# Kernel optimization log

Measured on AMD Instinct MI355X. Metric: run time of the kernel, lower is better.

## Reference

```python
import jax, jax.numpy as jnp
import numpy as np

M, D, I, E, TOPK = 2048, 1024, 2048, 8, 2

def setup_inputs() -> dict:
    key = jax.random.key(0)
    k1, k2, k3, k4 = jax.random.split(key, 4)
    x = jax.random.normal(k1, (M, D), dtype=jnp.float32)
    w13 = jax.random.normal(k2, (E, 2 * I, D), dtype=jnp.float32) * 0.02
    w2 = jax.random.normal(k3, (E, D, I), dtype=jnp.float32) * 0.02
    expert_indices = jax.random.randint(k4, (M, TOPK), 0, E, dtype=jnp.int64)
    return {"x": x, "w13": w13, "w2": w2, "expert_indices": expert_indices}

def reference(x, w13, w2, expert_indices):
    # Faithful to the 'gpt-fast' math: per (token, slot) SiLU-gated expert FFN.
    # Instead of gathering per-token weight copies (huge), compute each expert's
    # FFN densely over all tokens, then gather the selected expert output.
    inter = w2.shape[2]

    def per_expert(w13_e, w2_e):
        h = jnp.einsum('md,nd->mn', x, w13_e)          # [M, 2I]
        x1, x3 = h[:, :inter], h[:, inter:]
        return jnp.einsum('mi,di->md', jax.nn.silu(x1) * x3, w2_e)  # [M, D]

    outs = jax.vmap(per_expert)(w13, w2)               # [E, M, D]
    outs = jnp.transpose(outs, (1, 0, 2))              # [M, E, D]
    # out[t, a] = outs[t, expert_indices[t, a]]
    idx = expert_indices[..., None]                    # [M, TOPK, 1]
    return jnp.take_along_axis(outs, idx, axis=1)      # [M, TOPK, D]
```

## Files before the change

kernel.cpp:

```cpp
#include <hip/hip_runtime.h>
#include <hip/hip_bf16.h>
#include <cstdint>
#include <cstddef>

#define DDIM  1024
#define IDIM  2048
#define NEXP  8
#define NPAIR 4096
#define KSPLIT 4
#define MAXTILE 40

typedef __attribute__((ext_vector_type(8))) short short8;
typedef __attribute__((ext_vector_type(4))) float floatx4;
typedef __attribute__((ext_vector_type(4))) float fvec4;

__device__ inline short8 pack8(float4 a, float4 b) {
    union { short8 s8; __hip_bfloat162 h[4]; } u;
    u.h[0] = __float22bfloat162_rn(float2{a.x, a.y});
    u.h[1] = __float22bfloat162_rn(float2{a.z, a.w});
    u.h[2] = __float22bfloat162_rn(float2{b.x, b.y});
    u.h[3] = __float22bfloat162_rn(float2{b.z, b.w});
    return u.s8;
}

__device__ inline short8 pack8v(fvec4 a, fvec4 b) {
    union { short8 s8; __hip_bfloat162 h[4]; } u;
    u.h[0] = __float22bfloat162_rn(float2{a.x, a.y});
    u.h[1] = __float22bfloat162_rn(float2{a.z, a.w});
    u.h[2] = __float22bfloat162_rn(float2{b.x, b.y});
    u.h[3] = __float22bfloat162_rn(float2{b.z, b.w});
    return u.s8;
}

__device__ inline void gload_lds16(const unsigned short* g, unsigned short* l) {
    __builtin_amdgcn_global_load_lds((const __attribute__((address_space(1))) void*)g,
                                     (__attribute__((address_space(3))) void*)l, 16, 0, 0);
}

__launch_bounds__(256)
__global__ void cvt_all(const fvec4* __restrict__ x, const fvec4* __restrict__ w13,
                        const fvec4* __restrict__ w2,
                        uint4* __restrict__ xb, uint4* __restrict__ w13b,
                        uint4* __restrict__ w2b) {
    const int t = threadIdx.x;
    for (int job = blockIdx.x; job < 6400; job += gridDim.x) {
        const fvec4* src; uint4* dst; int cbase;
        if (job < 4096)      { src = w13; dst = w13b; cbase = job << 10; }
        else if (job < 6144) { src = w2;  dst = w2b;  cbase = (job - 4096) << 10; }
        else                 { src = x;   dst = xb;   cbase = (job - 6144) << 10; }
        const int c0 = cbase + t;
        fvec4 a0 = __builtin_nontemporal_load(src + 2 * (c0 + 0));
        fvec4 b0 = __builtin_nontemporal_load(src + 2 * (c0 + 0) + 1);
        fvec4 a1 = __builtin_nontemporal_load(src + 2 * (c0 + 256));
        fvec4 b1 = __builtin_nontemporal_load(src + 2 * (c0 + 256) + 1);
        fvec4 a2 = __builtin_nontemporal_load(src + 2 * (c0 + 512));
        fvec4 b2 = __builtin_nontemporal_load(src + 2 * (c0 + 512) + 1);
        fvec4 a3 = __builtin_nontemporal_load(src + 2 * (c0 + 768));
        fvec4 b3 = __builtin_nontemporal_load(src + 2 * (c0 + 768) + 1);
        __builtin_amdgcn_sched_barrier(0);
        short8 p0 = pack8v(a0, b0);
        short8 p1 = pack8v(a1, b1);
        short8 p2 = pack8v(a2, b2);
        short8 p3 = pack8v(a3, b3);
        dst[c0 + 0]   = *(uint4*)&p0;
        dst[c0 + 256] = *(uint4*)&p1;
        dst[c0 + 512] = *(uint4*)&p2;
        dst[c0 + 768] = *(uint4*)&p3;
    }
}

__global__ void route_kernel(const int* __restrict__ eidx,
                             int4* __restrict__ tbl,
                             int* __restrict__ slot_q) {
    __shared__ int cnt[NEXP];
    __shared__ int cur[NEXP];
    const int t = threadIdx.x;
    if (t < NEXP) cnt[t] = 0;
    __syncthreads();
    for (int q = t; q < NPAIR; q += 1024) atomicAdd(&cnt[eidx[q]], 1);
    __syncthreads();
    if (t == 0) {
        int s = 0, nt = 0;
        for (int e = 0; e < NEXP; e++) {
            cur[e] = s;
            for (int mb = 0; mb < cnt[e]; mb += 128)
                tbl[nt++] = int4{e, mb, s, cnt[e]};
            s += cnt[e];
        }
        for (; nt < MAXTILE; nt++) tbl[nt] = int4{0, 0, 0, 0};
    }
    __syncthreads();
    for (int q = t; q < NPAIR; q += 1024) {
        int e = eidx[q];
        int pos = atomicAdd(&cur[e], 1);
        slot_q[pos] = q;
    }
}

__launch_bounds__(256)
__global__ void gemm1_swiglu(const unsigned short* __restrict__ xb,
                             const unsigned short* __restrict__ w13b,
                             const int4* __restrict__ tbl,
                             const int* __restrict__ slot_q,
                             unsigned short* __restrict__ pbuf) {
    const int4 tt = tbl[blockIdx.y];
    const int e = tt.x, mbase = tt.y, off0 = tt.z, ne = tt.w;
    if (mbase >= ne) return;
    const int n0 = blockIdx.x * 64;

    __shared__ __align__(16) unsigned short As[128 * 64];
    __shared__ __align__(16) unsigned short Bs[128 * 64];

    const int t    = threadIdx.x;
    const int lane = t & 63;
    const int wid  = t >> 6;

    const int rr = t >> 3;
    const int g  = (t & 7) ^ (rr & 7);
    const unsigned short* pA[4];
    const unsigned short* pB[4];
    const unsigned short* wb1 = w13b + (size_t)e * (2 * IDIM) * DDIM;
    #pragma unroll
    for (int c = 0; c < 4; c++) {
        int row = c * 32 + rr;
        int sl = mbase + row; if (sl > ne - 1) sl = ne - 1;
        pA[c] = xb + (size_t)(slot_q[off0 + sl] >> 1) * DDIM + g * 8;
        int wrow = (row < 64) ? (n0 + row) : (IDIM + n0 + (row - 64));
        pB[c] = wb1 + (size_t)wrow * DDIM + g * 8;
    }
    unsigned short* lA = As + wid * 512;
    unsigned short* lB = Bs + wid * 512;

    const int wm = wid >> 1, wn = wid & 1;
    const int quad = lane >> 4, l16 = lane & 15;
    const int rsw = l16 & 7;
    const int co0 = (quad ^ rsw) * 8;
    const int co1 = ((quad + 4) ^ rsw) * 8;

    floatx4 acc1[4][2], acc3[4][2];
    #pragma unroll
    for (int i = 0; i < 4; i++)
        #pragma unroll
        for (int j = 0; j < 2; j++) {
            acc1[i][j] = floatx4{0.f, 0.f, 0.f, 0.f};
            acc3[i][j] = floatx4{0.f, 0.f, 0.f, 0.f};
        }

    for (int it = 0; it < DDIM / 64; ++it) {
        const int ko = it * 64;
        __syncthreads();
        #pragma unroll
        for (int c = 0; c < 4; c++) {
            gload_lds16(pA[c] + ko, lA + c * 2048);
            gload_lds16(pB[c] + ko, lB + c * 2048);
        }
        __syncthreads();

        #pragma unroll
        for (int h = 0; h < 2; ++h) {
            const int co = h ? co1 : co0;
            short8 af[4], b1f[2], b3f[2];
            #pragma unroll
            for (int mi = 0; mi < 4; mi++)
                af[mi] = *(short8*)&As[(wm * 64 + mi * 16 + l16) * 64 + co];
            #pragma unroll
            for (int ni = 0; ni < 2; ni++) {
                b1f[ni] = *(short8*)&Bs[(wn * 32 + ni * 16 + l16) * 64 + co];
                b3f[ni] = *(short8*)&Bs[(64 + wn * 32 + ni * 16 + l16) * 64 + co];
            }
            #pragma unroll
            for (int mi = 0; mi < 4; mi++)
                #pragma unroll
                for (int ni = 0; ni < 2; ni++) {
                    acc1[mi][ni] = __builtin_amdgcn_mfma_f32_16x16x32_bf16(af[mi], b1f[ni], acc1[mi][ni], 0, 0, 0);
                    acc3[mi][ni] = __builtin_amdgcn_mfma_f32_16x16x32_bf16(af[mi], b3f[ni], acc3[mi][ni], 0, 0, 0);
                }
        }
    }

    #pragma unroll
    for (int mi = 0; mi < 4; mi++) {
        #pragma unroll
        for (int ni = 0; ni < 2; ni++) {
            const int col = n0 + wn * 32 + ni * 16 + l16;
            #pragma unroll
            for (int rw = 0; rw < 4; rw++) {
                const int s2 = mbase + wm * 64 + mi * 16 + quad * 4 + rw;
                if (s2 < ne) {
                    float v1 = acc1[mi][ni][rw];
                    float v3 = acc3[mi][ni][rw];
                    float pv = v1 / (1.f + __expf(-v1)) * v3;
                    __hip_bfloat16 pb = __float2bfloat16(pv);
                    pbuf[(size_t)(off0 + s2) * IDIM + col] = *(unsigned short*)&pb;
                }
            }
        }
    }
}

__launch_bounds__(256)
__global__ void gemm2_scatter(const unsigned short* __restrict__ pbuf,
                              const unsigned short* __restrict__ w2b,
                              const int4* __restrict__ tbl,
                              const int* __restrict__ slot_q,
                              float* __restrict__ parts) {
    const int4 tt = tbl[blockIdx.y];
    const int e = tt.x, mbase = tt.y, off0 = tt.z, ne = tt.w;
    if (mbase >= ne) return;
    const int n0 = blockIdx.x * 128;
    const int kbase = blockIdx.z * (IDIM / KSPLIT);
    float* dstbase = parts + (size_t)blockIdx.z * NPAIR * DDIM;

    __shared__ __align__(16) unsigned short As[128 * 64];
    __shared__ __align__(16) unsigned short Bs[128 * 64];

    const int t    = threadIdx.x;
    const int lane = t & 63;
    const int wid  = t >> 6;

    const int rr = t >> 3;
    const int g  = (t & 7) ^ (rr & 7);
    const unsigned short* pA[4];
    const unsigned short* pB[4];
    const unsigned short* wb = w2b + (size_t)e * DDIM * IDIM;
    #pragma unroll
    for (int c = 0; c < 4; c++) {
        int row = c * 32 + rr;
        int sl = mbase + row; if (sl > ne - 1) sl = ne - 1;
        pA[c] = pbuf + (size_t)(off0 + sl) * IDIM + kbase + g * 8;
        pB[c] = wb + (size_t)(n0 + row) * IDIM + kbase + g * 8;
    }
    unsigned short* lA = As + wid * 512;
    unsigned short* lB = Bs + wid * 512;

    const int wm = wid >> 1, wn = wid & 1;
    const int quad = lane >> 4, l16 = lane & 15;
    const int rsw = l16 & 7;
    const int co0 = (quad ^ rsw) * 8;
    const int co1 = ((quad + 4) ^ rsw) * 8;

    floatx4 acc[4][4];
    #pragma unroll
    for (int i = 0; i < 4; i++)
        #pragma unroll
        for (int j = 0; j < 4; j++) acc[i][j] = floatx4{0.f, 0.f, 0.f, 0.f};

    for (int it = 0; it < (IDIM / KSPLIT) / 64; ++it) {
        const int ko = it * 64;
        __syncthreads();
        #pragma unroll
        for (int c = 0; c < 4; c++) {
            gload_lds16(pA[c] + ko, lA + c * 2048);
            gload_lds16(pB[c] + ko, lB + c * 2048);
        }
        __syncthreads();

        #pragma unroll
        for (int h = 0; h < 2; ++h) {
            const int co = h ? co1 : co0;
            short8 af[4], bf[4];
            #pragma unroll
            for (int mi = 0; mi < 4; mi++)
                af[mi] = *(short8*)&As[(wm * 64 + mi * 16 + l16) * 64 + co];
            #pragma unroll
            for (int ni = 0; ni < 4; ni++)
                bf[ni] = *(short8*)&Bs[(wn * 64 + ni * 16 + l16) * 64 + co];
            #pragma unroll
            for (int mi = 0; mi < 4; mi++)
                #pragma unroll
                for (int ni = 0; ni < 4; ni++)
                    acc[mi][ni] = __builtin_amdgcn_mfma_f32_16x16x32_bf16(af[mi], bf[ni], acc[mi][ni], 0, 0, 0);
        }
    }

    #pragma unroll
    for (int mi = 0; mi < 4; mi++) {
        #pragma unroll
        for (int rw = 0; rw < 4; rw++) {
            const int s2 = mbase + wm * 64 + mi * 16 + quad * 4 + rw;
            if (s2 < ne) {
                const int qq = slot_q[off0 + s2];
                float* orow = dstbase + (size_t)qq * DDIM;
                #pragma unroll
                for (int ni = 0; ni < 4; ni++)
                    orow[n0 + wn * 64 + ni * 16 + l16] = acc[mi][ni][rw];
            }
        }
    }
}

__global__ void reduce_add4(float4* __restrict__ out, const float4* __restrict__ parts) {
    const int i = blockIdx.x * 256 + threadIdx.x;
    const int stride = NPAIR * DDIM / 4;
    float4 a = parts[i], b = parts[i + stride];
    float4 c = parts[i + 2 * stride], d = parts[i + 3 * stride];
    out[i] = float4{a.x + b.x + c.x + d.x, a.y + b.y + c.y + d.y,
                    a.z + b.z + c.z + d.z, a.w + b.w + c.w + d.w};
}

extern "C" void kernel_launch(void* const* d_in, const int* in_sizes, int n_in,
                              void* d_out, int out_size, void* d_ws, size_t ws_size,
                              hipStream_t stream) {
    const float* x    = (const float*)d_in[0];
    const float* w13  = (const float*)d_in[1];
    const float* w2   = (const float*)d_in[2];
    const int*   eidx = (const int*)d_in[3];
    float* out = (float*)d_out;

    const size_t OFF_XB   = 65536;
    const size_t OFF_W13B = OFF_XB + (size_t)4 * 1024 * 1024;
    const size_t OFF_W2B  = OFF_W13B + (size_t)64 * 1024 * 1024;
    const size_t OFF_PBUF = OFF_W2B + (size_t)32 * 1024 * 1024;

    int4* tbl   = (int4*)((char*)d_ws + 128);
    int* slot_q = (int*)((char*)d_ws + 1024);
    unsigned short* xb   = (unsigned short*)((char*)d_ws + OFF_XB);
    unsigned short* w13b = (unsigned short*)((char*)d_ws + OFF_W13B);
    unsigned short* w2b  = (unsigned short*)((char*)d_ws + OFF_W2B);
    unsigned short* pbuf = (unsigned short*)((char*)d_ws + OFF_PBUF);
    float* parts = (float*)((char*)d_ws + OFF_W13B);

    hipLaunchKernelGGL(route_kernel, dim3(1), dim3(1024), 0, stream, eidx, tbl, slot_q);
    hipLaunchKernelGGL(cvt_all, dim3(6400), dim3(256), 0, stream,
                       (const fvec4*)x, (const fvec4*)w13, (const fvec4*)w2,
                       (uint4*)xb, (uint4*)w13b, (uint4*)w2b);
    hipLaunchKernelGGL(gemm1_swiglu, dim3(IDIM / 64, MAXTILE), dim3(256), 0, stream,
                       xb, w13b, tbl, slot_q, pbuf);
    hipLaunchKernelGGL(gemm2_scatter, dim3(DDIM / 128, MAXTILE, KSPLIT), dim3(256), 0, stream,
                       pbuf, w2b, tbl, slot_q, parts);
    hipLaunchKernelGGL(reduce_add4, dim3((NPAIR * DDIM / 4) / 256), dim3(256), 0, stream,
                       (float4*)out, (const float4*)parts);
}
```

Measured before the change: 360.1 us.

## Drop split-K in second GEMM, write output directly with narrower N tiles

Removes the 4-way K split of the down-projection GEMM, along with its fp32 partial buffers and the separate reduction kernel. Each block now covers the full K range over a 64-wide N tile and scatters results straight into the output. This avoids writing and re-reading about 64 MB of partial sums and saves one launch. In exchange each block runs a K loop four times longer, the grid has half as many blocks as the old split-K grid, and B-tile reuse per block drops.

```diff
diff --git a/kernel.cpp b/kernel.cpp
--- a/kernel.cpp
+++ b/kernel.cpp
@@ -7,21 +7,11 @@
 #define IDIM  2048
 #define NEXP  8
 #define NPAIR 4096
-#define KSPLIT 4
 #define MAXTILE 40
 
 typedef __attribute__((ext_vector_type(8))) short short8;
 typedef __attribute__((ext_vector_type(4))) float floatx4;
 typedef __attribute__((ext_vector_type(4))) float fvec4;
-
-__device__ inline short8 pack8(float4 a, float4 b) {
-    union { short8 s8; __hip_bfloat162 h[4]; } u;
-    u.h[0] = __float22bfloat162_rn(float2{a.x, a.y});
-    u.h[1] = __float22bfloat162_rn(float2{a.z, a.w});
-    u.h[2] = __float22bfloat162_rn(float2{b.x, b.y});
-    u.h[3] = __float22bfloat162_rn(float2{b.z, b.w});
-    return u.s8;
-}
 
 __device__ inline short8 pack8v(fvec4 a, fvec4 b) {
     union { short8 s8; __hip_bfloat162 h[4]; } u;
@@ -199,20 +189,18 @@
 }
 
 __launch_bounds__(256)
-__global__ void gemm2_scatter(const unsigned short* __restrict__ pbuf,
-                              const unsigned short* __restrict__ w2b,
-                              const int4* __restrict__ tbl,
-                              const int* __restrict__ slot_q,
-                              float* __restrict__ parts) {
+__global__ void gemm2_out(const unsigned short* __restrict__ pbuf,
+                          const unsigned short* __restrict__ w2b,
+                          const int4* __restrict__ tbl,
+                          const int* __restrict__ slot_q,
+                          float* __restrict__ out) {
     const int4 tt = tbl[blockIdx.y];
     const int e = tt.x, mbase = tt.y, off0 = tt.z, ne = tt.w;
     if (mbase >= ne) return;
-    const int n0 = blockIdx.x * 128;
-    const int kbase = blockIdx.z * (IDIM / KSPLIT);
-    float* dstbase = parts + (size_t)blockIdx.z * NPAIR * DDIM;
+    const int n0 = blockIdx.x * 64;
 
     __shared__ __align__(16) unsigned short As[128 * 64];
-    __shared__ __align__(16) unsigned short Bs[128 * 64];
+    __shared__ __align__(16) unsigned short Bs[64 * 64];
 
     const int t    = threadIdx.x;
     const int lane = t & 63;
@@ -221,14 +209,18 @@
     const int rr = t >> 3;
     const int g  = (t & 7) ^ (rr & 7);
     const unsigned short* pA[4];
-    const unsigned short* pB[4];
+    const unsigned short* pB[2];
     const unsigned short* wb = w2b + (size_t)e * DDIM * IDIM;
     #pragma unroll
     for (int c = 0; c < 4; c++) {
         int row = c * 32 + rr;
         int sl = mbase + row; if (sl > ne - 1) sl = ne - 1;
-        pA[c] = pbuf + (size_t)(off0 + sl) * IDIM + kbase + g * 8;
-        pB[c] = wb + (size_t)(n0 + row) * IDIM + kbase + g * 8;
+        pA[c] = pbuf + (size_t)(off0 + sl) * IDIM + g * 8;
+    }
+    #pragma unroll
+    for (int c = 0; c < 2; c++) {
+        int row = c * 32 + rr;
+        pB[c] = wb + (size_t)(n0 + row) * IDIM + g * 8;
     }
     unsigned short* lA = As + wid * 512;
     unsigned short* lB = Bs + wid * 512;
@@ -239,36 +231,37 @@
     const int co0 = (quad ^ rsw) * 8;
     const int co1 = ((quad + 4) ^ rsw) * 8;
 
-    floatx4 acc[4][4];
+    floatx4 acc[4][2];
     #pragma unroll
     for (int i = 0; i < 4; i++)
         #pragma unroll
-        for (int j = 0; j < 4; j++) acc[i][j] = floatx4{0.f, 0.f, 0.f, 0.f};
-
-    for (int it = 0; it < (IDIM / KSPLIT) / 64; ++it) {
+        for (int j = 0; j < 2; j++) acc[i][j] = floatx4{0.f, 0.f, 0.f, 0.f};
+
+    for (int it = 0; it < IDIM / 64; ++it) {
         const int ko = it * 64;
         __syncthreads();
         #pragma unroll
-        for (int c = 0; c < 4; c++) {
+        for (int c = 0; c < 4; c++)
             gload_lds16(pA[c] + ko, lA + c * 2048);
+        #pragma unroll
+        for (int c = 0; c < 2; c++)
             gload_lds16(pB[c] + ko, lB + c * 2048);
-        }
         __syncthreads();
 
         #pragma unroll
         for (int h = 0; h < 2; ++h) {
             const int co = h ? co1 : co0;
-            short8 af[4], bf[4];
+            short8 af[4], bf[2];
             #pragma unroll
             for (int mi = 0; mi < 4; mi++)
                 af[mi] = *(short8*)&As[(wm * 64 + mi * 16 + l16) * 64 + co];
             #pragma unroll
-            for (int ni = 0; ni < 4; ni++)
-                bf[ni] = *(short8*)&Bs[(wn * 64 + ni * 16 + l16) * 64 + co];
+            for (int ni = 0; ni < 2; ni++)
+                bf[ni] = *(short8*)&Bs[(wn * 32 + ni * 16 + l16) * 64 + co];
             #pragma unroll
             for (int mi = 0; mi < 4; mi++)
                 #pragma unroll
-                for (int ni = 0; ni < 4; ni++)
+                for (int ni = 0; ni < 2; ni++)
                     acc[mi][ni] = __builtin_amdgcn_mfma_f32_16x16x32_bf16(af[mi], bf[ni], acc[mi][ni], 0, 0, 0);
         }
     }
@@ -280,22 +273,13 @@
             const int s2 = mbase + wm * 64 + mi * 16 + quad * 4 + rw;
             if (s2 < ne) {
                 const int qq = slot_q[off0 + s2];
-                float* orow = dstbase + (size_t)qq * DDIM;
+                float* orow = out + (size_t)qq * DDIM;
                 #pragma unroll
-                for (int ni = 0; ni < 4; ni++)
-                    orow[n0 + wn * 64 + ni * 16 + l16] = acc[mi][ni][rw];
+                for (int ni = 0; ni < 2; ni++)
+                    orow[n0 + wn * 32 + ni * 16 + l16] = acc[mi][ni][rw];
             }
         }
     }
-}
-
-__global__ void reduce_add4(float4* __restrict__ out, const float4* __restrict__ parts) {
-    const int i = blockIdx.x * 256 + threadIdx.x;
-    const int stride = NPAIR * DDIM / 4;
-    float4 a = parts[i], b = parts[i + stride];
-    float4 c = parts[i + 2 * stride], d = parts[i + 3 * stride];
-    out[i] = float4{a.x + b.x + c.x + d.x, a.y + b.y + c.y + d.y,
-                    a.z + b.z + c.z + d.z, a.w + b.w + c.w + d.w};
 }
 
 extern "C" void kernel_launch(void* const* d_in, const int* in_sizes, int n_in,
@@ -318,7 +302,6 @@
     unsigned short* w13b = (unsigned short*)((char*)d_ws + OFF_W13B);
     unsigned short* w2b  = (unsigned short*)((char*)d_ws + OFF_W2B);
     unsigned short* pbuf = (unsigned short*)((char*)d_ws + OFF_PBUF);
-    float* parts = (float*)((char*)d_ws + OFF_W13B);
 
     hipLaunchKernelGGL(route_kernel, dim3(1), dim3(1024), 0, stream, eidx, tbl, slot_q);
     hipLaunchKernelGGL(cvt_all, dim3(6400), dim3(256), 0, stream,
@@ -326,8 +309,6 @@
                        (uint4*)xb, (uint4*)w13b, (uint4*)w2b);
     hipLaunchKernelGGL(gemm1_swiglu, dim3(IDIM / 64, MAXTILE), dim3(256), 0, stream,
                        xb, w13b, tbl, slot_q, pbuf);
-    hipLaunchKernelGGL(gemm2_scatter, dim3(DDIM / 128, MAXTILE, KSPLIT), dim3(256), 0, stream,
-                       pbuf, w2b, tbl, slot_q, parts);
-    hipLaunchKernelGGL(reduce_add4, dim3((NPAIR * DDIM / 4) / 256), dim3(256), 0, stream,
-                       (float4*)out, (const float4*)parts);
-}
+    hipLaunchKernelGGL(gemm2_out, dim3(DDIM / 64, MAXTILE), dim3(256), 0, stream,
+                       pbuf, w2b, tbl, slot_q, out);
+}
```

New measurement: 342.7 us. -4.9%, faster.
